# Optimization experiments

Hardware: AMD Instinct MI355X
Metric: run time of the kernel (lower is better)

## Reference

```python
import jax, jax.numpy as jnp
import numpy as np

E = 2048      # embed_dim
H = 32        # num_heads
G = 8         # group_num
HD = E // H   # head_dim = 64
HPG = H // G  # heads per group = 4


def setup_inputs() -> dict:
    key = jax.random.key(0)
    ks = jax.random.split(key, 9)
    s = 0.02
    return {
        "x": jax.random.normal(ks[0], (1, 2048, E), dtype=jnp.float32),
        "Wq": jax.random.normal(ks[1], (E, E), dtype=jnp.float32) * s,
        "bq": jnp.zeros((E,), dtype=jnp.float32),
        "Wk": jax.random.normal(ks[2], (G * HD, E), dtype=jnp.float32) * s,
        "bk": jnp.zeros((G * HD,), dtype=jnp.float32),
        "Wv": jax.random.normal(ks[3], (G * HD, E), dtype=jnp.float32) * s,
        "bv": jnp.zeros((G * HD,), dtype=jnp.float32),
        "Wo": jax.random.normal(ks[4], (E, E), dtype=jnp.float32) * s,
        "bo": jnp.zeros((E,), dtype=jnp.float32),
    }


def reference(x, Wq, bq, Wk, bk, Wv, bv, Wo, bo):
    B, S, _ = x.shape
    # projections (torch Linear: y = x @ W.T + b)
    q = x @ Wq.T + bq                                   # [B,S,E]
    k = x @ Wk.T + bk                                   # [B,S,G*HD]
    v = x @ Wv.T + bv                                   # [B,S,G*HD]
    # [B,S,H,HD] -> [B,H,S,HD] -> [B,G,HPG,S,HD]
    q = q.reshape(B, S, H, HD).transpose(0, 2, 1, 3).reshape(B, G, HPG, S, HD)
    k = k.reshape(B, S, G, HD).transpose(0, 2, 1, 3)    # [B,G,S,HD]
    v = v.reshape(B, S, G, HD).transpose(0, 2, 1, 3)    # [B,G,S,HD]
    scale = 1.0 / np.float32(np.sqrt(HD))
    scores = jnp.einsum('bgnsh,bgth->bgnst', q, k) * scale   # [B,G,HPG,S,S]
    attn = jax.nn.softmax(scores, axis=-1)
    out = jnp.einsum('bgnst,bgth->bgnsh', attn, v)           # [B,G,HPG,S,HD]
    out = out.reshape(B, H, S, HD).transpose(0, 2, 1, 3).reshape(B, S, E)
    out = out @ Wo.T + bo
    attn_weights = attn.reshape(B, H, S, S)
    return (attn_weights, out)
```

## Files before the change

### kernel.cpp

```cpp
#include <hip/hip_runtime.h>
#include <stdint.h>

#define S_LEN 2048
#define EMB   2048
#define NHEAD 32
#define HDIM  64
#define QKVN  3072
#define KOFF  2048
#define VOFF  2560

typedef __attribute__((ext_vector_type(8))) short short8;
typedef __attribute__((ext_vector_type(4))) short short4v;
typedef __attribute__((ext_vector_type(4))) float f32x4;

__device__ __forceinline__ unsigned short f2bf(float f) {
  union { float f; unsigned u; } v; v.f = f;
  return (unsigned short)((v.u + 0x7fffu + ((v.u >> 16) & 1u)) >> 16);
}

__device__ __forceinline__ f32x4 mfma16(short8 a, short8 b, f32x4 c) {
  return __builtin_amdgcn_mfma_f32_16x16x32_bf16(a, b, c, 0, 0, 0);
}

__device__ __forceinline__ void gload_lds16(const void* g, void* l) {
  __builtin_amdgcn_global_load_lds(
      (const __attribute__((address_space(1))) void*)g,
      (__attribute__((address_space(3))) void*)l, 16, 0, 0);
}

__device__ __forceinline__ unsigned cvt_pk_bf16(float lo, float hi) {
  unsigned r;
  asm("v_cvt_pk_bf16_f32 %0, %1, %2" : "=v"(r) : "v"(lo), "v"(hi));
  return r;
}

__device__ __forceinline__ float bperm_f32(int idx_bytes, float v) {
  int r = __builtin_amdgcn_ds_bpermute(idx_bytes, __builtin_bit_cast(int, v));
  return __builtin_bit_cast(float, r);
}

__device__ __forceinline__ float bf16lo_f32(unsigned u) {
  return __builtin_bit_cast(float, u << 16);
}
__device__ __forceinline__ float bf16hi_f32(unsigned u) {
  return __builtin_bit_cast(float, u & 0xffff0000u);
}

__global__ __launch_bounds__(256) void k_cvt_all(
    const float* __restrict__ x, const float* __restrict__ Wq,
    const float* __restrict__ Wk, const float* __restrict__ Wv,
    const float* __restrict__ Wo, unsigned short* __restrict__ xb,
    unsigned short* __restrict__ wqkv, unsigned short* __restrict__ wob) {
  long i = (long)(blockIdx.x * blockDim.x + threadIdx.x) * 4;
  const float* src; unsigned short* dst; long off;
  if (i < 4194304L)       { src = x;  dst = xb;             off = i; }
  else if (i < 8388608L)  { src = Wq; dst = wqkv;           off = i - 4194304L; }
  else if (i < 9437184L)  { src = Wk; dst = wqkv + 4194304; off = i - 8388608L; }
  else if (i < 10485760L) { src = Wv; dst = wqkv + 5242880; off = i - 9437184L; }
  else                    { src = Wo; dst = wob;            off = i - 10485760L; }
  float4 v = *reinterpret_cast<const float4*>(src + off);
  short4v o;
  o.x = (short)f2bf(v.x); o.y = (short)f2bf(v.y);
  o.z = (short)f2bf(v.z); o.w = (short)f2bf(v.w);
  *reinterpret_cast<short4v*>(dst + off) = o;
}

__global__ void k_bias_cat(const float* __restrict__ bq, const float* __restrict__ bk,
                           const float* __restrict__ bv, float* __restrict__ dst) {
  int i = blockIdx.x * blockDim.x + threadIdx.x;
  if (i < 2048) dst[i] = bq[i];
  else if (i < 2560) dst[i] = bk[i - 2048];
  else dst[i] = bv[i - 2560];
}

template <typename OUT_T>
__global__ __launch_bounds__(256) void k_gemm_bt(
    const unsigned short* __restrict__ A, const unsigned short* __restrict__ B,
    const float* __restrict__ bias, OUT_T* __restrict__ C, int M, int N, int K) {
  __shared__ unsigned short As[128 * 32];
  __shared__ unsigned short Bs[128 * 32];
  const int t = threadIdx.x;
  const int l = t & 63;
  const int w = t >> 6;
  const int m0 = blockIdx.x * 128;
  const int n0 = blockIdx.y * 128;
  const int wm = w >> 1, wn = w & 1;

  f32x4 acc[4][4] = {};

  const unsigned short* ga0 = A + (size_t)(m0 + (t >> 2)) * K + (t & 3) * 8;
  const unsigned short* ga1 = ga0 + (size_t)64 * K;
  const unsigned short* gb0 = B + (size_t)(n0 + (t >> 2)) * K + (t & 3) * 8;
  const unsigned short* gb1 = gb0 + (size_t)64 * K;
  unsigned short* la0 = As + t * 8;
  unsigned short* la1 = As + 2048 + t * 8;
  unsigned short* lb0 = Bs + t * 8;
  unsigned short* lb1 = Bs + 2048 + t * 8;

  const int lr = l & 15;
  const int lk = (l >> 4) * 8;
  const unsigned short* arow = As + (wm * 64 + lr) * 32 + lk;
  const unsigned short* brow = Bs + (wn * 64 + lr) * 32 + lk;

  for (int k0 = 0; k0 < K; k0 += 32) {
    gload_lds16(ga0, la0);
    gload_lds16(ga1, la1);
    gload_lds16(gb0, lb0);
    gload_lds16(gb1, lb1);
    ga0 += 32; ga1 += 32; gb0 += 32; gb1 += 32;
    __syncthreads();
    short8 af[4], bfv[4];
#pragma unroll
    for (int i = 0; i < 4; i++) {
      af[i]  = *reinterpret_cast<const short8*>(arow + i * 16 * 32);
      bfv[i] = *reinterpret_cast<const short8*>(brow + i * 16 * 32);
    }
#pragma unroll
    for (int i = 0; i < 4; i++)
#pragma unroll
      for (int j = 0; j < 4; j++)
        acc[i][j] = mfma16(af[i], bfv[j], acc[i][j]);
    __syncthreads();
  }

  const int lg = l >> 4;
#pragma unroll
  for (int i = 0; i < 4; i++) {
#pragma unroll
    for (int j = 0; j < 4; j++) {
      int col = n0 + wn * 64 + j * 16 + lr;
      float bb = bias[col];
#pragma unroll
      for (int r = 0; r < 4; r++) {
        int row = m0 + wm * 64 + i * 16 + lg * 4 + r;
        float val = acc[i][j][r] + bb;
        if constexpr (sizeof(OUT_T) == 2)
          C[(size_t)row * N + col] = (OUT_T)f2bf(val);
        else
          C[(size_t)row * N + col] = (OUT_T)val;
      }
    }
  }
}

__global__ __launch_bounds__(256) void k_kc(const unsigned short* __restrict__ qkv,
                                            unsigned short* __restrict__ kc) {
  const int gi = blockIdx.x >> 4;
  const int c  = blockIdx.x & 15;
  const int t = threadIdx.x;
  const int row = t & 127;
  const int part = t >> 7;
  const unsigned short* src =
      qkv + (size_t)(c * 128 + row) * QKVN + KOFF + gi * 64 + part * 32;
  char* dst = (char*)kc + ((size_t)(gi * 16 + c) << 14);
  const int swz = (row & 7) << 4;
#pragma unroll
  for (int j = 0; j < 4; ++j) {
    short8 v = *reinterpret_cast<const short8*>(src + j * 8);
    int b = (row * 128 + part * 64 + j * 16) ^ swz;
    *reinterpret_cast<short8*>(dst + b) = v;
  }
}

__global__ __launch_bounds__(256) void k_vT(const unsigned short* __restrict__ qkv,
                                            unsigned short* __restrict__ vt) {
  __shared__ unsigned short tile[64][72];
  const int t = threadIdx.x;
  const int p0 = (blockIdx.x & 31) * 64;
  const int g0 = (blockIdx.x >> 5) * 64;
  {
    const int pl = t >> 3;
    const int gl = (t & 7) * 8;
#pragma unroll
    for (int i = 0; i < 2; i++) {
      int p = pl + i * 32;
      short8 v = *reinterpret_cast<const short8*>(qkv + (size_t)(p0 + p) * QKVN + VOFF + g0 + gl);
#pragma unroll
      for (int j = 0; j < 8; j++) tile[p][gl + j] = (unsigned short)v[j];
    }
  }
  __syncthreads();
  {
    const int gr = t >> 3;
    const int pc = (t & 7) * 8;
    const int cb = pc & ~31;
    const int rbase = pc & 31;
    const int chunk = p0 >> 7;
    const int colin = (p0 & 64) + pc;
    const int grp = g0 >> 6;
#pragma unroll
    for (int i = 0; i < 2; i++) {
      int g = gr + i * 32;
      short8 o;
#pragma unroll
      for (int j = 0; j < 8; j++) {
        int rp = rbase + j;
        int q8 = rp >> 3, jj = rp & 7;
        int src = cb + ((jj < 4) ? (q8 * 4 + jj) : (16 + q8 * 4 + (jj - 4)));
        o[j] = (short)tile[src][g];
      }
      int b = (g * 256 + colin * 2) ^ ((g & 7) << 4);
      *reinterpret_cast<short8*>(
          (char*)vt + (((size_t)(grp * 16 + chunk)) << 14) + b) = o;
    }
  }
}

__global__ __launch_bounds__(512, 4) void k_attn(
    const unsigned short* __restrict__ qkv, const unsigned short* __restrict__ kc,
    const unsigned short* __restrict__ vt, float* __restrict__ attn_w,
    unsigned short* __restrict__ hout) {
  __shared__ unsigned short Kt[8192];
  __shared__ unsigned short Vt[8192];
  const int t = threadIdx.x;
  const int l = t & 63;
  const int w = t >> 6;
  const int g = blockIdx.x & 7;
  const int bi = blockIdx.x >> 3;
  const int unit = bi * 8 + w;
  const int h = g * 4 + (unit & 3);
  const int r0 = (unit >> 2) * 16;
  const int lr = l & 15;
  const int lg = l >> 4;
  const int lk = lg * 8;
  const int swz = (lr & 7) << 4;

  const unsigned short* qbase = qkv + (size_t)(r0 + lr) * QKVN + h * HDIM + lk;
  const short8 bq0 = *reinterpret_cast<const short8*>(qbase);
  const short8 bq1 = *reinterpret_cast<const short8*>(qbase + 32);

  const char* kcg = (const char*)kc + ((size_t)(g * 16) << 14);
  const char* vtg = (const char*)vt + ((size_t)(g * 16) << 14);
  char* kdst = (char*)Kt;
  char* vdst = (char*)Vt;
  const char* kldb = (const char*)Kt;
  const char* vldb = (const char*)Vt;

#define STAGE_K(c)                                                      \
  { const char* s_ = kcg + ((size_t)(c) << 14);                         \
    gload_lds16(s_ + t * 16, kdst + t * 16);                            \
    gload_lds16(s_ + 8192 + t * 16, kdst + 8192 + t * 16); }
#define STAGE_V(c)                                                      \
  { const char* s_ = vtg + ((size_t)(c) << 14);                         \
    gload_lds16(s_ + t * 16, vdst + t * 16);                            \
    gload_lds16(s_ + 8192 + t * 16, vdst + 8192 + t * 16); }
#define LGKM_BAR()                                                      \
  asm volatile("s_waitcnt lgkmcnt(0)\n\ts_barrier" ::: "memory");       \
  __builtin_amdgcn_sched_barrier(0);

  float m = -1e30f, sm = 0.f;
  STAGE_K(0);
  __syncthreads();
  for (int c = 0; c < 16; ++c) {
    f32x4 acc[8];
#pragma unroll
    for (int i = 0; i < 8; ++i) {
      int rb = ((i * 16 + lr) << 7) + (lg << 4);
      short8 a0 = *reinterpret_cast<const short8*>(kldb + (rb ^ swz));
      short8 a1 = *reinterpret_cast<const short8*>(kldb + ((rb + 64) ^ swz));
      f32x4 a = {};
      a = mfma16(a0, bq0, a);
      a = mfma16(a1, bq1, a);
      acc[i] = a * 0.125f;
    }
    float mc = -1e30f;
#pragma unroll
    for (int i = 0; i < 8; ++i)
      mc = fmaxf(mc, fmaxf(fmaxf(acc[i][0], acc[i][1]), fmaxf(acc[i][2], acc[i][3])));
    mc = fmaxf(mc, __shfl_xor(mc, 16, 64));
    mc = fmaxf(mc, __shfl_xor(mc, 32, 64));
    float nm = fmaxf(m, mc);
    float ps = 0.f;
#pragma unroll
    for (int i = 0; i < 8; ++i) {
#pragma unroll
      for (int r = 0; r < 4; ++r) ps += __expf(acc[i][r] - nm);
    }
    ps += __shfl_xor(ps, 16, 64);
    ps += __shfl_xor(ps, 32, 64);
    sm = sm * __expf(m - nm) + ps;
    m = nm;
    LGKM_BAR();
    if (c < 15) STAGE_K(c + 1);
    __syncthreads();
  }
  const float inv = 1.0f / sm;

  f32x4 pv0 = {}, pv1 = {}, pv2 = {}, pv3 = {};
  const int jj = l & 7;
  const int rown = l >> 3;
  const int idx0 = ((l & 3) * 16 + rown) * 4;
  const int idx1 = idx0 + 32;
  const bool hiq = (l & 4) != 0;
  float* arow0 = attn_w + (size_t)h * S_LEN * S_LEN
               + (size_t)(r0 + rown) * S_LEN + jj * 4;
  float* arow1 = arow0 + 8 * S_LEN;

  STAGE_K(0);
  STAGE_V(0);
  __syncthreads();
  for (int c = 0; c < 16; ++c) {
    const int kcol = c * 128;
    union A8 { short8 s; unsigned u[4]; } pa8[4];
#pragma unroll
    for (int i = 0; i < 8; ++i) {
      int rb = ((i * 16 + lr) << 7) + (lg << 4);
      short8 a0 = *reinterpret_cast<const short8*>(kldb + (rb ^ swz));
      short8 a1 = *reinterpret_cast<const short8*>(kldb + ((rb + 64) ^ swz));
      f32x4 a = {};
      a = mfma16(a0, bq0, a);
      a = mfma16(a1, bq1, a);
      float p0 = __expf(a[0] * 0.125f - m) * inv;
      float p1 = __expf(a[1] * 0.125f - m) * inv;
      float p2 = __expf(a[2] * 0.125f - m) * inv;
      float p3 = __expf(a[3] * 0.125f - m) * inv;
      pa8[i >> 1].u[(i & 1) * 2 + 0] = cvt_pk_bf16(p0, p1);
      pa8[i >> 1].u[(i & 1) * 2 + 1] = cvt_pk_bf16(p2, p3);
    }
#pragma unroll
    for (int s = 0; s < 4; ++s) {
      f32x4 X, Y;
      X[0] = bf16lo_f32(pa8[s].u[0]); X[1] = bf16hi_f32(pa8[s].u[0]);
      X[2] = bf16lo_f32(pa8[s].u[1]); X[3] = bf16hi_f32(pa8[s].u[1]);
      Y[0] = bf16lo_f32(pa8[s].u[2]); Y[1] = bf16hi_f32(pa8[s].u[2]);
      Y[2] = bf16lo_f32(pa8[s].u[3]); Y[3] = bf16hi_f32(pa8[s].u[3]);
      f32x4 o0, o1;
#pragma unroll
      for (int cc = 0; cc < 4; ++cc) {
        float x0 = bperm_f32(idx0, X[cc]);
        float y0 = bperm_f32(idx0, Y[cc]);
        o0[cc] = hiq ? y0 : x0;
        float x1 = bperm_f32(idx1, X[cc]);
        float y1 = bperm_f32(idx1, Y[cc]);
        o1[cc] = hiq ? y1 : x1;
      }
      __builtin_nontemporal_store(o0, reinterpret_cast<f32x4*>(arow0 + kcol + s * 32));
      __builtin_nontemporal_store(o1, reinterpret_cast<f32x4*>(arow1 + kcol + s * 32));
    }
#pragma unroll
    for (int s = 0; s < 4; ++s) {
      int cbyte = s * 64 + (lg << 4);
      short8 b0 = *reinterpret_cast<const short8*>(vldb + ((((lr) << 8) + cbyte) ^ swz));
      short8 b1 = *reinterpret_cast<const short8*>(vldb + ((((16 + lr) << 8) + cbyte) ^ swz));
      short8 b2 = *reinterpret_cast<const short8*>(vldb + ((((32 + lr) << 8) + cbyte) ^ swz));
      short8 b3 = *reinterpret_cast<const short8*>(vldb + ((((48 + lr) << 8) + cbyte) ^ swz));
      pv0 = mfma16(pa8[s].s, b0, pv0);
      pv1 = mfma16(pa8[s].s, b1, pv1);
      pv2 = mfma16(pa8[s].s, b2, pv2);
      pv3 = mfma16(pa8[s].s, b3, pv3);
    }
    LGKM_BAR();
    if (c < 15) { STAGE_K(c + 1); STAGE_V(c + 1); }
    __syncthreads();
  }

  unsigned short* hb = hout + (size_t)(r0 + lg * 4) * EMB + h * HDIM + lr;
#pragma unroll
  for (int r = 0; r < 4; ++r) {
    hb[(size_t)r * EMB +  0] = f2bf(pv0[r]);
    hb[(size_t)r * EMB + 16] = f2bf(pv1[r]);
    hb[(size_t)r * EMB + 32] = f2bf(pv2[r]);
    hb[(size_t)r * EMB + 48] = f2bf(pv3[r]);
  }
#undef STAGE_K
#undef STAGE_V
#undef LGKM_BAR
}

extern "C" void kernel_launch(void* const* d_in, const int* in_sizes, int n_in,
                              void* d_out, int out_size, void* d_ws, size_t ws_size,
                              hipStream_t stream) {
  const float* x  = (const float*)d_in[0];
  const float* Wq = (const float*)d_in[1];
  const float* bq = (const float*)d_in[2];
  const float* Wk = (const float*)d_in[3];
  const float* bk = (const float*)d_in[4];
  const float* Wv = (const float*)d_in[5];
  const float* bv = (const float*)d_in[6];
  const float* Wo = (const float*)d_in[7];
  const float* bo = (const float*)d_in[8];
  float* out = (float*)d_out;

  char* ws = (char*)d_ws;
  unsigned short* x_bf  = (unsigned short*)(ws);
  unsigned short* wqkv  = (unsigned short*)(ws + (8ull  << 20));
  unsigned short* wo_bf = (unsigned short*)(ws + (20ull << 20));
  float*          bqkv  = (float*)         (ws + (28ull << 20));
  unsigned short* qkv   = (unsigned short*)(ws + (29ull << 20));
  unsigned short* vt_b  = (unsigned short*)(ws + (41ull << 20));
  unsigned short* hout  = (unsigned short*)(ws + (43ull << 20));
  unsigned short* kc_b  = (unsigned short*)(ws + (51ull << 20));

  k_cvt_all<<<14336, 256, 0, stream>>>(x, Wq, Wk, Wv, Wo, x_bf, wqkv, wo_bf);
  k_bias_cat<<<12, 256, 0, stream>>>(bq, bk, bv, bqkv);

  dim3 g1(16, 24);
  k_gemm_bt<unsigned short><<<g1, 256, 0, stream>>>(x_bf, wqkv, bqkv, qkv, 2048, 3072, 2048);
  k_kc<<<128, 256, 0, stream>>>(qkv, kc_b);
  k_vT<<<256, 256, 0, stream>>>(qkv, vt_b);
  k_attn<<<512, 512, 0, stream>>>(qkv, kc_b, vt_b, out, hout);
  dim3 g2(16, 16);
  k_gemm_bt<float><<<g2, 256, 0, stream>>>(hout, wo_bf, bo, out + (size_t)NHEAD * S_LEN * S_LEN, 2048, 2048, 2048);
}
```

Before: 330.1 us.

## Process two query tiles per wave with double-buffered K/V staging in attention

Each wave now computes 32 query rows (two 16-row tiles) against every K/V fragment read from LDS, so each shared-memory read feeds twice the MFMA work. The block shrinks to 256 threads and K/V staging becomes double-buffered, so the next chunk's global-to-LDS load is issued before the current chunk is computed and can overlap with it. The ds_bpermute transpose and nontemporal stores for the attention-weight output are dropped in favour of direct 16-byte stores in MFMA layout. In exchange it needs more registers per wave and uses a less contiguous store pattern for the large attention matrix, which could cost write bandwidth.

Result: slower. 376.0 us (+13.9%).

```diff
diff --git a/kernel.cpp b/kernel.cpp
--- a/kernel.cpp
+++ b/kernel.cpp
@@ -32,11 +32,6 @@
   unsigned r;
   asm("v_cvt_pk_bf16_f32 %0, %1, %2" : "=v"(r) : "v"(lo), "v"(hi));
   return r;
-}
-
-__device__ __forceinline__ float bperm_f32(int idx_bytes, float v) {
-  int r = __builtin_amdgcn_ds_bpermute(idx_bytes, __builtin_bit_cast(int, v));
-  return __builtin_bit_cast(float, r);
 }
 
 __device__ __forceinline__ float bf16lo_f32(unsigned u) {
@@ -206,165 +201,193 @@
   }
 }
 
-__global__ __launch_bounds__(512, 4) void k_attn(
+__global__ __launch_bounds__(256, 2) void k_attn(
     const unsigned short* __restrict__ qkv, const unsigned short* __restrict__ kc,
     const unsigned short* __restrict__ vt, float* __restrict__ attn_w,
     unsigned short* __restrict__ hout) {
-  __shared__ unsigned short Kt[8192];
-  __shared__ unsigned short Vt[8192];
+  __shared__ unsigned short Kt[2][8192];
+  __shared__ unsigned short Vt[2][8192];
   const int t = threadIdx.x;
   const int l = t & 63;
   const int w = t >> 6;
   const int g = blockIdx.x & 7;
   const int bi = blockIdx.x >> 3;
-  const int unit = bi * 8 + w;
-  const int h = g * 4 + (unit & 3);
-  const int r0 = (unit >> 2) * 16;
+  const int u = bi * 4 + w;
+  const int h = g * 4 + (u & 3);
+  const int r0 = (u >> 2) * 32;
   const int lr = l & 15;
   const int lg = l >> 4;
   const int lk = lg * 8;
   const int swz = (lr & 7) << 4;
 
-  const unsigned short* qbase = qkv + (size_t)(r0 + lr) * QKVN + h * HDIM + lk;
-  const short8 bq0 = *reinterpret_cast<const short8*>(qbase);
-  const short8 bq1 = *reinterpret_cast<const short8*>(qbase + 32);
+  const unsigned short* qA = qkv + (size_t)(r0 + lr) * QKVN + h * HDIM + lk;
+  const unsigned short* qB = qA + (size_t)16 * QKVN;
+  const short8 bqA0 = *reinterpret_cast<const short8*>(qA);
+  const short8 bqA1 = *reinterpret_cast<const short8*>(qA + 32);
+  const short8 bqB0 = *reinterpret_cast<const short8*>(qB);
+  const short8 bqB1 = *reinterpret_cast<const short8*>(qB + 32);
 
   const char* kcg = (const char*)kc + ((size_t)(g * 16) << 14);
   const char* vtg = (const char*)vt + ((size_t)(g * 16) << 14);
-  char* kdst = (char*)Kt;
-  char* vdst = (char*)Vt;
-  const char* kldb = (const char*)Kt;
-  const char* vldb = (const char*)Vt;
-
-#define STAGE_K(c)                                                      \
-  { const char* s_ = kcg + ((size_t)(c) << 14);                         \
-    gload_lds16(s_ + t * 16, kdst + t * 16);                            \
-    gload_lds16(s_ + 8192 + t * 16, kdst + 8192 + t * 16); }
-#define STAGE_V(c)                                                      \
-  { const char* s_ = vtg + ((size_t)(c) << 14);                         \
-    gload_lds16(s_ + t * 16, vdst + t * 16);                            \
-    gload_lds16(s_ + 8192 + t * 16, vdst + 8192 + t * 16); }
-#define LGKM_BAR()                                                      \
-  asm volatile("s_waitcnt lgkmcnt(0)\n\ts_barrier" ::: "memory");       \
-  __builtin_amdgcn_sched_barrier(0);
-
-  float m = -1e30f, sm = 0.f;
-  STAGE_K(0);
+
+#define STAGE_K(c, b)                                                     \
+  { const char* s_ = kcg + ((size_t)(c) << 14);                           \
+    char* d_ = (char*)Kt[b];                                              \
+    _Pragma("unroll")                                                     \
+    for (int j_ = 0; j_ < 4; ++j_)                                        \
+      gload_lds16(s_ + j_ * 4096 + t * 16, d_ + j_ * 4096 + t * 16); }
+#define STAGE_V(c, b)                                                     \
+  { const char* s_ = vtg + ((size_t)(c) << 14);                           \
+    char* d_ = (char*)Vt[b];                                              \
+    _Pragma("unroll")                                                     \
+    for (int j_ = 0; j_ < 4; ++j_)                                        \
+      gload_lds16(s_ + j_ * 4096 + t * 16, d_ + j_ * 4096 + t * 16); }
+
+  float mA = -1e30f, smA = 0.f, mB = -1e30f, smB = 0.f;
+  STAGE_K(0, 0);
   __syncthreads();
   for (int c = 0; c < 16; ++c) {
-    f32x4 acc[8];
+    if (c < 15) STAGE_K(c + 1, (c + 1) & 1);
+    const char* kb = (const char*)Kt[c & 1];
+    f32x4 aA[8], aB[8];
 #pragma unroll
     for (int i = 0; i < 8; ++i) {
       int rb = ((i * 16 + lr) << 7) + (lg << 4);
-      short8 a0 = *reinterpret_cast<const short8*>(kldb + (rb ^ swz));
-      short8 a1 = *reinterpret_cast<const short8*>(kldb + ((rb + 64) ^ swz));
-      f32x4 a = {};
-      a = mfma16(a0, bq0, a);
-      a = mfma16(a1, bq1, a);
-      acc[i] = a * 0.125f;
-    }
-    float mc = -1e30f;
-#pragma unroll
-    for (int i = 0; i < 8; ++i)
-      mc = fmaxf(mc, fmaxf(fmaxf(acc[i][0], acc[i][1]), fmaxf(acc[i][2], acc[i][3])));
-    mc = fmaxf(mc, __shfl_xor(mc, 16, 64));
-    mc = fmaxf(mc, __shfl_xor(mc, 32, 64));
-    float nm = fmaxf(m, mc);
-    float ps = 0.f;
+      short8 a0 = *reinterpret_cast<const short8*>(kb + (rb ^ swz));
+      short8 a1 = *reinterpret_cast<const short8*>(kb + ((rb + 64) ^ swz));
+      f32x4 x = {};
+      x = mfma16(a0, bqA0, x);
+      x = mfma16(a1, bqA1, x);
+      aA[i] = x * 0.125f;
+      f32x4 y = {};
+      y = mfma16(a0, bqB0, y);
+      y = mfma16(a1, bqB1, y);
+      aB[i] = y * 0.125f;
+    }
+    float mcA = -1e30f, mcB = -1e30f;
 #pragma unroll
     for (int i = 0; i < 8; ++i) {
-#pragma unroll
-      for (int r = 0; r < 4; ++r) ps += __expf(acc[i][r] - nm);
-    }
-    ps += __shfl_xor(ps, 16, 64);
-    ps += __shfl_xor(ps, 32, 64);
-    sm = sm * __expf(m - nm) + ps;
-    m = nm;
-    LGKM_BAR();
-    if (c < 15) STAGE_K(c + 1);
+      mcA = fmaxf(mcA, fmaxf(fmaxf(aA[i][0], aA[i][1]), fmaxf(aA[i][2], aA[i][3])));
+      mcB = fmaxf(mcB, fmaxf(fmaxf(aB[i][0], aB[i][1]), fmaxf(aB[i][2], aB[i][3])));
+    }
+    mcA = fmaxf(mcA, __shfl_xor(mcA, 16, 64));
+    mcA = fmaxf(mcA, __shfl_xor(mcA, 32, 64));
+    mcB = fmaxf(mcB, __shfl_xor(mcB, 16, 64));
+    mcB = fmaxf(mcB, __shfl_xor(mcB, 32, 64));
+    float nmA = fmaxf(mA, mcA);
+    float nmB = fmaxf(mB, mcB);
+    float psA = 0.f, psB = 0.f;
+#pragma unroll
+    for (int i = 0; i < 8; ++i) {
+#pragma unroll
+      for (int r = 0; r < 4; ++r) {
+        psA += __expf(aA[i][r] - nmA);
+        psB += __expf(aB[i][r] - nmB);
+      }
+    }
+    psA += __shfl_xor(psA, 16, 64);
+    psA += __shfl_xor(psA, 32, 64);
+    psB += __shfl_xor(psB, 16, 64);
+    psB += __shfl_xor(psB, 32, 64);
+    smA = smA * __expf(mA - nmA) + psA;
+    smB = smB * __expf(mB - nmB) + psB;
+    mA = nmA; mB = nmB;
     __syncthreads();
   }
-  const float inv = 1.0f / sm;
-
-  f32x4 pv0 = {}, pv1 = {}, pv2 = {}, pv3 = {};
-  const int jj = l & 7;
-  const int rown = l >> 3;
-  const int idx0 = ((l & 3) * 16 + rown) * 4;
-  const int idx1 = idx0 + 32;
-  const bool hiq = (l & 4) != 0;
-  float* arow0 = attn_w + (size_t)h * S_LEN * S_LEN
-               + (size_t)(r0 + rown) * S_LEN + jj * 4;
-  float* arow1 = arow0 + 8 * S_LEN;
-
-  STAGE_K(0);
-  STAGE_V(0);
+  const float invA = 1.0f / smA;
+  const float invB = 1.0f / smB;
+
+  f32x4 pvA0 = {}, pvA1 = {}, pvA2 = {}, pvA3 = {};
+  f32x4 pvB0 = {}, pvB1 = {}, pvB2 = {}, pvB3 = {};
+  float* aoutA = attn_w + (size_t)h * S_LEN * S_LEN + (size_t)(r0 + lr) * S_LEN;
+  float* aoutB = aoutA + (size_t)16 * S_LEN;
+
+  STAGE_K(0, 0);
+  STAGE_V(0, 0);
   __syncthreads();
   for (int c = 0; c < 16; ++c) {
+    const char* kb = (const char*)Kt[c & 1];
+    const char* vb = (const char*)Vt[c & 1];
     const int kcol = c * 128;
-    union A8 { short8 s; unsigned u[4]; } pa8[4];
+    union A8 { short8 s; unsigned u[4]; } paA[4], paB[4];
 #pragma unroll
     for (int i = 0; i < 8; ++i) {
       int rb = ((i * 16 + lr) << 7) + (lg << 4);
-      short8 a0 = *reinterpret_cast<const short8*>(kldb + (rb ^ swz));
-      short8 a1 = *reinterpret_cast<const short8*>(kldb + ((rb + 64) ^ swz));
-      f32x4 a = {};
-      a = mfma16(a0, bq0, a);
-      a = mfma16(a1, bq1, a);
-      float p0 = __expf(a[0] * 0.125f - m) * inv;
-      float p1 = __expf(a[1] * 0.125f - m) * inv;
-      float p2 = __expf(a[2] * 0.125f - m) * inv;
-      float p3 = __expf(a[3] * 0.125f - m) * inv;
-      pa8[i >> 1].u[(i & 1) * 2 + 0] = cvt_pk_bf16(p0, p1);
-      pa8[i >> 1].u[(i & 1) * 2 + 1] = cvt_pk_bf16(p2, p3);
-    }
+      short8 a0 = *reinterpret_cast<const short8*>(kb + (rb ^ swz));
+      short8 a1 = *reinterpret_cast<const short8*>(kb + ((rb + 64) ^ swz));
+      f32x4 x = {};
+      x = mfma16(a0, bqA0, x);
+      x = mfma16(a1, bqA1, x);
+      f32x4 y = {};
+      y = mfma16(a0, bqB0, y);
+      y = mfma16(a1, bqB1, y);
+      float pA0 = __expf(x[0] * 0.125f - mA) * invA;
+      float pA1 = __expf(x[1] * 0.125f - mA) * invA;
+      float pA2 = __expf(x[2] * 0.125f - mA) * invA;
+      float pA3 = __expf(x[3] * 0.125f - mA) * invA;
+      paA[i >> 1].u[(i & 1) * 2 + 0] = cvt_pk_bf16(pA0, pA1);
+      paA[i >> 1].u[(i & 1) * 2 + 1] = cvt_pk_bf16(pA2, pA3);
+      float pB0 = __expf(y[0] * 0.125f - mB) * invB;
+      float pB1 = __expf(y[1] * 0.125f - mB) * invB;
+      float pB2 = __expf(y[2] * 0.125f - mB) * invB;
+      float pB3 = __expf(y[3] * 0.125f - mB) * invB;
+      paB[i >> 1].u[(i & 1) * 2 + 0] = cvt_pk_bf16(pB0, pB1);
+      paB[i >> 1].u[(i & 1) * 2 + 1] = cvt_pk_bf16(pB2, pB3);
+    }
+    if (c < 15) { STAGE_K(c + 1, (c + 1) & 1); STAGE_V(c + 1, (c + 1) & 1); }
 #pragma unroll
     for (int s = 0; s < 4; ++s) {
       f32x4 X, Y;
-      X[0] = bf16lo_f32(pa8[s].u[0]); X[1] = bf16hi_f32(pa8[s].u[0]);
-      X[2] = bf16lo_f32(pa8[s].u[1]); X[3] = bf16hi_f32(pa8[s].u[1]);
-      Y[0] = bf16lo_f32(pa8[s].u[2]); Y[1] = bf16hi_f32(pa8[s].u[2]);
-      Y[2] = bf16lo_f32(pa8[s].u[3]); Y[3] = bf16hi_f32(pa8[s].u[3]);
-      f32x4 o0, o1;
-#pragma unroll
-      for (int cc = 0; cc < 4; ++cc) {
-        float x0 = bperm_f32(idx0, X[cc]);
-        float y0 = bperm_f32(idx0, Y[cc]);
-        o0[cc] = hiq ? y0 : x0;
-        float x1 = bperm_f32(idx1, X[cc]);
-        float y1 = bperm_f32(idx1, Y[cc]);
-        o1[cc] = hiq ? y1 : x1;
-      }
-      __builtin_nontemporal_store(o0, reinterpret_cast<f32x4*>(arow0 + kcol + s * 32));
-      __builtin_nontemporal_store(o1, reinterpret_cast<f32x4*>(arow1 + kcol + s * 32));
+      X[0] = bf16lo_f32(paA[s].u[0]); X[1] = bf16hi_f32(paA[s].u[0]);
+      X[2] = bf16lo_f32(paA[s].u[1]); X[3] = bf16hi_f32(paA[s].u[1]);
+      Y[0] = bf16lo_f32(paA[s].u[2]); Y[1] = bf16hi_f32(paA[s].u[2]);
+      Y[2] = bf16lo_f32(paA[s].u[3]); Y[3] = bf16hi_f32(paA[s].u[3]);
+      *reinterpret_cast<f32x4*>(aoutA + kcol + s * 32 + lg * 4) = X;
+      *reinterpret_cast<f32x4*>(aoutA + kcol + s * 32 + 16 + lg * 4) = Y;
+      X[0] = bf16lo_f32(paB[s].u[0]); X[1] = bf16hi_f32(paB[s].u[0]);
+      X[2] = bf16lo_f32(paB[s].u[1]); X[3] = bf16hi_f32(paB[s].u[1]);
+      Y[0] = bf16lo_f32(paB[s].u[2]); Y[1] = bf16hi_f32(paB[s].u[2]);
+      Y[2] = bf16lo_f32(paB[s].u[3]); Y[3] = bf16hi_f32(paB[s].u[3]);
+      *reinterpret_cast<f32x4*>(aoutB + kcol + s * 32 + lg * 4) = X;
+      *reinterpret_cast<f32x4*>(aoutB + kcol + s * 32 + 16 + lg * 4) = Y;
     }
 #pragma unroll
     for (int s = 0; s < 4; ++s) {
       int cbyte = s * 64 + (lg << 4);
-      short8 b0 = *reinterpret_cast<const short8*>(vldb + ((((lr) << 8) + cbyte) ^ swz));
-      short8 b1 = *reinterpret_cast<const short8*>(vldb + ((((16 + lr) << 8) + cbyte) ^ swz));
-      short8 b2 = *reinterpret_cast<const short8*>(vldb + ((((32 + lr) << 8) + cbyte) ^ swz));
-      short8 b3 = *reinterpret_cast<const short8*>(vldb + ((((48 + lr) << 8) + cbyte) ^ swz));
-      pv0 = mfma16(pa8[s].s, b0, pv0);
-      pv1 = mfma16(pa8[s].s, b1, pv1);
-      pv2 = mfma16(pa8[s].s, b2, pv2);
-      pv3 = mfma16(pa8[s].s, b3, pv3);
-    }
-    LGKM_BAR();
-    if (c < 15) { STAGE_K(c + 1); STAGE_V(c + 1); }
-    __syncthreads();
-  }
-
-  unsigned short* hb = hout + (size_t)(r0 + lg * 4) * EMB + h * HDIM + lr;
+      short8 b0 = *reinterpret_cast<const short8*>(vb + ((((lr) << 8) + cbyte) ^ swz));
+      short8 b1 = *reinterpret_cast<const short8*>(vb + ((((16 + lr) << 8) + cbyte) ^ swz));
+      short8 b2 = *reinterpret_cast<const short8*>(vb + ((((32 + lr) << 8) + cbyte) ^ swz));
+      short8 b3 = *reinterpret_cast<const short8*>(vb + ((((48 + lr) << 8) + cbyte) ^ swz));
+      pvA0 = mfma16(paA[s].s, b0, pvA0);
+      pvA1 = mfma16(paA[s].s, b1, pvA1);
+      pvA2 = mfma16(paA[s].s, b2, pvA2);
+      pvA3 = mfma16(paA[s].s, b3, pvA3);
+      pvB0 = mfma16(paB[s].s, b0, pvB0);
+      pvB1 = mfma16(paB[s].s, b1, pvB1);
+      pvB2 = mfma16(paB[s].s, b2, pvB2);
+      pvB3 = mfma16(paB[s].s, b3, pvB3);
+    }
+    if (c < 15) {
+      asm volatile("s_waitcnt vmcnt(16) lgkmcnt(0)\n\ts_barrier" ::: "memory");
+      __builtin_amdgcn_sched_barrier(0);
+    }
+  }
+
+  unsigned short* hbA = hout + (size_t)(r0 + lg * 4) * EMB + h * HDIM + lr;
+  unsigned short* hbB = hbA + (size_t)16 * EMB;
 #pragma unroll
   for (int r = 0; r < 4; ++r) {
-    hb[(size_t)r * EMB +  0] = f2bf(pv0[r]);
-    hb[(size_t)r * EMB + 16] = f2bf(pv1[r]);
-    hb[(size_t)r * EMB + 32] = f2bf(pv2[r]);
-    hb[(size_t)r * EMB + 48] = f2bf(pv3[r]);
+    hbA[(size_t)r * EMB +  0] = f2bf(pvA0[r]);
+    hbA[(size_t)r * EMB + 16] = f2bf(pvA1[r]);
+    hbA[(size_t)r * EMB + 32] = f2bf(pvA2[r]);
+    hbA[(size_t)r * EMB + 48] = f2bf(pvA3[r]);
+    hbB[(size_t)r * EMB +  0] = f2bf(pvB0[r]);
+    hbB[(size_t)r * EMB + 16] = f2bf(pvB1[r]);
+    hbB[(size_t)r * EMB + 32] = f2bf(pvB2[r]);
+    hbB[(size_t)r * EMB + 48] = f2bf(pvB3[r]);
   }
 #undef STAGE_K
 #undef STAGE_V
-#undef LGKM_BAR
 }
 
 extern "C" void kernel_launch(void* const* d_in, const int* in_sizes, int n_in,
@@ -398,7 +421,7 @@
   k_gemm_bt<unsigned short><<<g1, 256, 0, stream>>>(x_bf, wqkv, bqkv, qkv, 2048, 3072, 2048);
   k_kc<<<128, 256, 0, stream>>>(qkv, kc_b);
   k_vT<<<256, 256, 0, stream>>>(qkv, vt_b);
-  k_attn<<<512, 512, 0, stream>>>(qkv, kc_b, vt_b, out, hout);
+  k_attn<<<512, 256, 0, stream>>>(qkv, kc_b, vt_b, out, hout);
   dim3 g2(16, 16);
   k_gemm_bt<float><<<g2, 256, 0, stream>>>(hout, wo_bf, bo, out + (size_t)NHEAD * S_LEN * S_LEN, 2048, 2048, 2048);
 }
```

## Double-buffer K/V LDS tiles and store attention weights directly from MFMA layout

Applied to the files above, without the earlier changes.

K and V tiles in LDS are now double-buffered so the next chunk's global-to-LDS load is issued before the current chunk is computed, with partial vmcnt waits replacing the full wait-then-stage barrier. The ds_bpermute-based transpose of the probability tile is removed; each lane writes its own 16-byte fragments straight to the attention-weights output in the MFMA accumulator layout, using plain instead of nontemporal stores. This cuts LDS permute traffic and exposed load latency. In exchange it doubles LDS per block, which likely lowers occupancy, and makes the large attention-weight write less contiguous per wavefront.

Result: slower. 355.2 us (+7.6%).

```diff
diff --git a/kernel.cpp b/kernel.cpp
--- a/kernel.cpp
+++ b/kernel.cpp
@@ -32,11 +32,6 @@
   unsigned r;
   asm("v_cvt_pk_bf16_f32 %0, %1, %2" : "=v"(r) : "v"(lo), "v"(hi));
   return r;
-}
-
-__device__ __forceinline__ float bperm_f32(int idx_bytes, float v) {
-  int r = __builtin_amdgcn_ds_bpermute(idx_bytes, __builtin_bit_cast(int, v));
-  return __builtin_bit_cast(float, r);
 }
 
 __device__ __forceinline__ float bf16lo_f32(unsigned u) {
@@ -210,8 +205,8 @@
     const unsigned short* __restrict__ qkv, const unsigned short* __restrict__ kc,
     const unsigned short* __restrict__ vt, float* __restrict__ attn_w,
     unsigned short* __restrict__ hout) {
-  __shared__ unsigned short Kt[8192];
-  __shared__ unsigned short Vt[8192];
+  __shared__ unsigned short Kt[2][8192];
+  __shared__ unsigned short Vt[2][8192];
   const int t = threadIdx.x;
   const int l = t & 63;
   const int w = t >> 6;
@@ -231,33 +226,30 @@
 
   const char* kcg = (const char*)kc + ((size_t)(g * 16) << 14);
   const char* vtg = (const char*)vt + ((size_t)(g * 16) << 14);
-  char* kdst = (char*)Kt;
-  char* vdst = (char*)Vt;
-  const char* kldb = (const char*)Kt;
-  const char* vldb = (const char*)Vt;
-
-#define STAGE_K(c)                                                      \
-  { const char* s_ = kcg + ((size_t)(c) << 14);                         \
-    gload_lds16(s_ + t * 16, kdst + t * 16);                            \
-    gload_lds16(s_ + 8192 + t * 16, kdst + 8192 + t * 16); }
-#define STAGE_V(c)                                                      \
-  { const char* s_ = vtg + ((size_t)(c) << 14);                         \
-    gload_lds16(s_ + t * 16, vdst + t * 16);                            \
-    gload_lds16(s_ + 8192 + t * 16, vdst + 8192 + t * 16); }
-#define LGKM_BAR()                                                      \
-  asm volatile("s_waitcnt lgkmcnt(0)\n\ts_barrier" ::: "memory");       \
-  __builtin_amdgcn_sched_barrier(0);
+
+#define STAGE_K(c, b)                                                    \
+  { const char* s_ = kcg + ((size_t)(c) << 14);                          \
+    char* d_ = (char*)Kt[b];                                             \
+    gload_lds16(s_ + t * 16, d_ + t * 16);                               \
+    gload_lds16(s_ + 8192 + t * 16, d_ + 8192 + t * 16); }
+#define STAGE_V(c, b)                                                    \
+  { const char* s_ = vtg + ((size_t)(c) << 14);                          \
+    char* d_ = (char*)Vt[b];                                             \
+    gload_lds16(s_ + t * 16, d_ + t * 16);                               \
+    gload_lds16(s_ + 8192 + t * 16, d_ + 8192 + t * 16); }
 
   float m = -1e30f, sm = 0.f;
-  STAGE_K(0);
+  STAGE_K(0, 0);
   __syncthreads();
   for (int c = 0; c < 16; ++c) {
+    if (c < 15) STAGE_K(c + 1, (c + 1) & 1);
+    const char* kb = (const char*)Kt[c & 1];
     f32x4 acc[8];
 #pragma unroll
     for (int i = 0; i < 8; ++i) {
       int rb = ((i * 16 + lr) << 7) + (lg << 4);
-      short8 a0 = *reinterpret_cast<const short8*>(kldb + (rb ^ swz));
-      short8 a1 = *reinterpret_cast<const short8*>(kldb + ((rb + 64) ^ swz));
+      short8 a0 = *reinterpret_cast<const short8*>(kb + (rb ^ swz));
+      short8 a1 = *reinterpret_cast<const short8*>(kb + ((rb + 64) ^ swz));
       f32x4 a = {};
       a = mfma16(a0, bq0, a);
       a = mfma16(a1, bq1, a);
@@ -280,33 +272,29 @@
     ps += __shfl_xor(ps, 32, 64);
     sm = sm * __expf(m - nm) + ps;
     m = nm;
-    LGKM_BAR();
-    if (c < 15) STAGE_K(c + 1);
-    __syncthreads();
+    if (c < 15) {
+      asm volatile("s_waitcnt vmcnt(0) lgkmcnt(0)\n\ts_barrier" ::: "memory");
+      __builtin_amdgcn_sched_barrier(0);
+    }
   }
   const float inv = 1.0f / sm;
 
   f32x4 pv0 = {}, pv1 = {}, pv2 = {}, pv3 = {};
-  const int jj = l & 7;
-  const int rown = l >> 3;
-  const int idx0 = ((l & 3) * 16 + rown) * 4;
-  const int idx1 = idx0 + 32;
-  const bool hiq = (l & 4) != 0;
-  float* arow0 = attn_w + (size_t)h * S_LEN * S_LEN
-               + (size_t)(r0 + rown) * S_LEN + jj * 4;
-  float* arow1 = arow0 + 8 * S_LEN;
-
-  STAGE_K(0);
-  STAGE_V(0);
+  float* aout = attn_w + (size_t)h * S_LEN * S_LEN + (size_t)(r0 + lr) * S_LEN;
+
+  STAGE_K(0, 0);
+  STAGE_V(0, 0);
   __syncthreads();
   for (int c = 0; c < 16; ++c) {
+    const char* kb = (const char*)Kt[c & 1];
+    const char* vb = (const char*)Vt[c & 1];
     const int kcol = c * 128;
     union A8 { short8 s; unsigned u[4]; } pa8[4];
 #pragma unroll
     for (int i = 0; i < 8; ++i) {
       int rb = ((i * 16 + lr) << 7) + (lg << 4);
-      short8 a0 = *reinterpret_cast<const short8*>(kldb + (rb ^ swz));
-      short8 a1 = *reinterpret_cast<const short8*>(kldb + ((rb + 64) ^ swz));
+      short8 a0 = *reinterpret_cast<const short8*>(kb + (rb ^ swz));
+      short8 a1 = *reinterpret_cast<const short8*>(kb + ((rb + 64) ^ swz));
       f32x4 a = {};
       a = mfma16(a0, bq0, a);
       a = mfma16(a1, bq1, a);
@@ -317,6 +305,7 @@
       pa8[i >> 1].u[(i & 1) * 2 + 0] = cvt_pk_bf16(p0, p1);
       pa8[i >> 1].u[(i & 1) * 2 + 1] = cvt_pk_bf16(p2, p3);
     }
+    if (c < 15) { STAGE_K(c + 1, (c + 1) & 1); STAGE_V(c + 1, (c + 1) & 1); }
 #pragma unroll
     for (int s = 0; s < 4; ++s) {
       f32x4 X, Y;
@@ -324,34 +313,25 @@
       X[2] = bf16lo_f32(pa8[s].u[1]); X[3] = bf16hi_f32(pa8[s].u[1]);
       Y[0] = bf16lo_f32(pa8[s].u[2]); Y[1] = bf16hi_f32(pa8[s].u[2]);
       Y[2] = bf16lo_f32(pa8[s].u[3]); Y[3] = bf16hi_f32(pa8[s].u[3]);
-      f32x4 o0, o1;
-#pragma unroll
-      for (int cc = 0; cc < 4; ++cc) {
-        float x0 = bperm_f32(idx0, X[cc]);
-        float y0 = bperm_f32(idx0, Y[cc]);
-        o0[cc] = hiq ? y0 : x0;
-        float x1 = bperm_f32(idx1, X[cc]);
-        float y1 = bperm_f32(idx1, Y[cc]);
-        o1[cc] = hiq ? y1 : x1;
-      }
-      __builtin_nontemporal_store(o0, reinterpret_cast<f32x4*>(arow0 + kcol + s * 32));
-      __builtin_nontemporal_store(o1, reinterpret_cast<f32x4*>(arow1 + kcol + s * 32));
+      *reinterpret_cast<f32x4*>(aout + kcol + s * 32 + lg * 4) = X;
+      *reinterpret_cast<f32x4*>(aout + kcol + s * 32 + 16 + lg * 4) = Y;
     }
 #pragma unroll
     for (int s = 0; s < 4; ++s) {
       int cbyte = s * 64 + (lg << 4);
-      short8 b0 = *reinterpret_cast<const short8*>(vldb + ((((lr) << 8) + cbyte) ^ swz));
-      short8 b1 = *reinterpret_cast<const short8*>(vldb + ((((16 + lr) << 8) + cbyte) ^ swz));
-      short8 b2 = *reinterpret_cast<const short8*>(vldb + ((((32 + lr) << 8) + cbyte) ^ swz));
-      short8 b3 = *reinterpret_cast<const short8*>(vldb + ((((48 + lr) << 8) + cbyte) ^ swz));
+      short8 b0 = *reinterpret_cast<const short8*>(vb + ((((lr) << 8) + cbyte) ^ swz));
+      short8 b1 = *reinterpret_cast<const short8*>(vb + ((((16 + lr) << 8) + cbyte) ^ swz));
+      short8 b2 = *reinterpret_cast<const short8*>(vb + ((((32 + lr) << 8) + cbyte) ^ swz));
+      short8 b3 = *reinterpret_cast<const short8*>(vb + ((((48 + lr) << 8) + cbyte) ^ swz));
       pv0 = mfma16(pa8[s].s, b0, pv0);
       pv1 = mfma16(pa8[s].s, b1, pv1);
       pv2 = mfma16(pa8[s].s, b2, pv2);
       pv3 = mfma16(pa8[s].s, b3, pv3);
     }
-    LGKM_BAR();
-    if (c < 15) { STAGE_K(c + 1); STAGE_V(c + 1); }
-    __syncthreads();
+    if (c < 15) {
+      asm volatile("s_waitcnt vmcnt(8) lgkmcnt(0)\n\ts_barrier" ::: "memory");
+      __builtin_amdgcn_sched_barrier(0);
+    }
   }
 
   unsigned short* hb = hout + (size_t)(r0 + lg * 4) * EMB + h * HDIM + lr;
@@ -364,7 +344,6 @@
   }
 #undef STAGE_K
 #undef STAGE_V
-#undef LGKM_BAR
 }
 
 extern "C" void kernel_launch(void* const* d_in, const int* in_sizes, int n_in,
```

## Drop bpermute transpose for attention-weight stores and overlap stores with staging

Applied to the files above, without the earlier changes.

Removes the ds_bpermute-based lane shuffle that transposed probabilities before writing the attention-weight matrix. Each lane now writes its own 16-byte chunks directly, using regular rather than nontemporal stores. The stores move after the next K/V staging is issued, and the end-of-iteration __syncthreads is replaced by a custom barrier that waits only on older memory ops (vmcnt(8)). The goal is to cut LDS/permute traffic and let the large attention-weight writes overlap with prefetch. The risk is less coalesced write patterns, the loss of the nontemporal hint, and the hand-tuned vmcnt being wrong for the actual number of outstanding loads.

Result: slower. 355.0 us (+7.5%).

```diff
diff --git a/kernel.cpp b/kernel.cpp
--- a/kernel.cpp
+++ b/kernel.cpp
@@ -32,11 +32,6 @@
   unsigned r;
   asm("v_cvt_pk_bf16_f32 %0, %1, %2" : "=v"(r) : "v"(lo), "v"(hi));
   return r;
-}
-
-__device__ __forceinline__ float bperm_f32(int idx_bytes, float v) {
-  int r = __builtin_amdgcn_ds_bpermute(idx_bytes, __builtin_bit_cast(int, v));
-  return __builtin_bit_cast(float, r);
 }
 
 __device__ __forceinline__ float bf16lo_f32(unsigned u) {
@@ -287,14 +282,7 @@
   const float inv = 1.0f / sm;
 
   f32x4 pv0 = {}, pv1 = {}, pv2 = {}, pv3 = {};
-  const int jj = l & 7;
-  const int rown = l >> 3;
-  const int idx0 = ((l & 3) * 16 + rown) * 4;
-  const int idx1 = idx0 + 32;
-  const bool hiq = (l & 4) != 0;
-  float* arow0 = attn_w + (size_t)h * S_LEN * S_LEN
-               + (size_t)(r0 + rown) * S_LEN + jj * 4;
-  float* arow1 = arow0 + 8 * S_LEN;
+  float* aout = attn_w + (size_t)h * S_LEN * S_LEN + (size_t)(r0 + lr) * S_LEN;
 
   STAGE_K(0);
   STAGE_V(0);
@@ -319,26 +307,6 @@
     }
 #pragma unroll
     for (int s = 0; s < 4; ++s) {
-      f32x4 X, Y;
-      X[0] = bf16lo_f32(pa8[s].u[0]); X[1] = bf16hi_f32(pa8[s].u[0]);
-      X[2] = bf16lo_f32(pa8[s].u[1]); X[3] = bf16hi_f32(pa8[s].u[1]);
-      Y[0] = bf16lo_f32(pa8[s].u[2]); Y[1] = bf16hi_f32(pa8[s].u[2]);
-      Y[2] = bf16lo_f32(pa8[s].u[3]); Y[3] = bf16hi_f32(pa8[s].u[3]);
-      f32x4 o0, o1;
-#pragma unroll
-      for (int cc = 0; cc < 4; ++cc) {
-        float x0 = bperm_f32(idx0, X[cc]);
-        float y0 = bperm_f32(idx0, Y[cc]);
-        o0[cc] = hiq ? y0 : x0;
-        float x1 = bperm_f32(idx1, X[cc]);
-        float y1 = bperm_f32(idx1, Y[cc]);
-        o1[cc] = hiq ? y1 : x1;
-      }
-      __builtin_nontemporal_store(o0, reinterpret_cast<f32x4*>(arow0 + kcol + s * 32));
-      __builtin_nontemporal_store(o1, reinterpret_cast<f32x4*>(arow1 + kcol + s * 32));
-    }
-#pragma unroll
-    for (int s = 0; s < 4; ++s) {
       int cbyte = s * 64 + (lg << 4);
       short8 b0 = *reinterpret_cast<const short8*>(vldb + ((((lr) << 8) + cbyte) ^ swz));
       short8 b1 = *reinterpret_cast<const short8*>(vldb + ((((16 + lr) << 8) + cbyte) ^ swz));
@@ -351,7 +319,20 @@
     }
     LGKM_BAR();
     if (c < 15) { STAGE_K(c + 1); STAGE_V(c + 1); }
-    __syncthreads();
+#pragma unroll
+    for (int s = 0; s < 4; ++s) {
+      f32x4 X, Y;
+      X[0] = bf16lo_f32(pa8[s].u[0]); X[1] = bf16hi_f32(pa8[s].u[0]);
+      X[2] = bf16lo_f32(pa8[s].u[1]); X[3] = bf16hi_f32(pa8[s].u[1]);
+      Y[0] = bf16lo_f32(pa8[s].u[2]); Y[1] = bf16hi_f32(pa8[s].u[2]);
+      Y[2] = bf16lo_f32(pa8[s].u[3]); Y[3] = bf16hi_f32(pa8[s].u[3]);
+      *reinterpret_cast<f32x4*>(aout + kcol + s * 32 + lg * 4) = X;
+      *reinterpret_cast<f32x4*>(aout + kcol + s * 32 + 16 + lg * 4) = Y;
+    }
+    if (c < 15) {
+      asm volatile("s_waitcnt vmcnt(8)\n\ts_barrier" ::: "memory");
+      __builtin_amdgcn_sched_barrier(0);
+    }
   }
 
   unsigned short* hb = hout + (size_t)(r0 + lg * 4) * EMB + h * HDIM + lr;
```
